# Performance work log

Hardware: AMD Instinct MI355X
Metric: run time of the kernel (lower is better)

The kernel has to match this reference:

```python
import jax, jax.numpy as jnp
import numpy as np


def setup_inputs() -> dict:
    key = jax.random.key(0)
    B, D = 256, 4096
    continuous_input = jax.random.normal(key, (B, D), dtype=jnp.float32)
    return {"continuous_input": continuous_input, "timesteps": 100}


def reference(continuous_input, timesteps):
    # Temporal coding: each (batch, input) pair fires exactly one spike at a
    # time determined by sigmoid(value). With num_neurons == input_dim the
    # neuron index is just the input index, so the scalar scatter in the
    # original nested Python loops is exactly a one-hot over the time axis.
    T = timesteps
    # torch .long() truncates; sigmoid*(T-1) >= 0 so floor == trunc
    spike_times = jnp.floor(jax.nn.sigmoid(continuous_input) * (T - 1)).astype(jnp.int32)  # [B, D]
    t = jnp.arange(T, dtype=jnp.int32)  # [T]
    spikes = (t[:, None, None] == spike_times[None, :, :]).astype(jnp.float32)  # [T, B, N]
    return spikes
```

## Files before the change

### kernel.cpp

```cpp
#include <hip/hip_runtime.h>
#include <math.h>


typedef __attribute__((ext_vector_type(4))) float f32x4;

__device__ __forceinline__ float sigmoidf(float x) {
    return 1.0f / (1.0f + expf(-x));
}

__global__ __launch_bounds__(256) void spike_time_kernel(
    const float* __restrict__ x, unsigned char* __restrict__ st,
    int n, float tm1) {
    const int e = (blockIdx.x * 256 + threadIdx.x) * 4;
    if (e + 3 < n) {
        f32x4 v = *reinterpret_cast<const f32x4*>(x + e);
        uchar4 s;
        s.x = (unsigned char)(int)(sigmoidf(v.x) * tm1);
        s.y = (unsigned char)(int)(sigmoidf(v.y) * tm1);
        s.z = (unsigned char)(int)(sigmoidf(v.z) * tm1);
        s.w = (unsigned char)(int)(sigmoidf(v.w) * tm1);
        *reinterpret_cast<uchar4*>(st + e) = s;
    } else {
        for (int i = e; i < n; ++i)
            st[i] = (unsigned char)(int)(sigmoidf(x[i]) * tm1);
    }
}

__global__ __launch_bounds__(256) void write_onehot_kernel(
    const unsigned char* __restrict__ st, float* __restrict__ out, int n) {
    const int t = blockIdx.y;
    const int e = (blockIdx.x * 256 + threadIdx.x) * 4;
    if (e + 3 < n) {
        uchar4 s = *reinterpret_cast<const uchar4*>(st + e);
        f32x4 o;
        o.x = (s.x == t) ? 1.0f : 0.0f;
        o.y = (s.y == t) ? 1.0f : 0.0f;
        o.z = (s.z == t) ? 1.0f : 0.0f;
        o.w = (s.w == t) ? 1.0f : 0.0f;
        *reinterpret_cast<f32x4*>(out + (size_t)t * n + e) = o;
    } else {
        for (int i = e; i < n; ++i)
            out[(size_t)t * n + i] = (st[i] == t) ? 1.0f : 0.0f;
    }
}

__global__ __launch_bounds__(256) void fused_onehot_kernel(
    const float* __restrict__ x, float* __restrict__ out, int n, float tm1) {
    const int t = blockIdx.y;
    const int e = (blockIdx.x * 256 + threadIdx.x) * 4;
    if (e + 3 < n) {
        f32x4 v = *reinterpret_cast<const f32x4*>(x + e);
        f32x4 o;
        o.x = ((int)(sigmoidf(v.x) * tm1) == t) ? 1.0f : 0.0f;
        o.y = ((int)(sigmoidf(v.y) * tm1) == t) ? 1.0f : 0.0f;
        o.z = ((int)(sigmoidf(v.z) * tm1) == t) ? 1.0f : 0.0f;
        o.w = ((int)(sigmoidf(v.w) * tm1) == t) ? 1.0f : 0.0f;
        *reinterpret_cast<f32x4*>(out + (size_t)t * n + e) = o;
    } else {
        for (int i = e; i < n; ++i)
            out[(size_t)t * n + i] = ((int)(sigmoidf(x[i]) * tm1) == t) ? 1.0f : 0.0f;
    }
}

extern "C" void kernel_launch(void* const* d_in, const int* in_sizes, int n_in,
                              void* d_out, int out_size, void* d_ws, size_t ws_size,
                              hipStream_t stream) {
    const float* x = (const float*)d_in[0];
    float* out = (float*)d_out;
    const int n = in_sizes[0];
    const int T = out_size / n;
    const float tm1 = (float)(T - 1);

    const int n4 = (n + 3) / 4;
    const int blocks_x = (n4 + 255) / 256;

    if (ws_size >= (size_t)n) {
        unsigned char* st = (unsigned char*)d_ws;
        spike_time_kernel<<<blocks_x, 256, 0, stream>>>(x, st, n, tm1);
        dim3 grid(blocks_x, T);
        write_onehot_kernel<<<grid, 256, 0, stream>>>(st, out, n);
    } else {
        dim3 grid(blocks_x, T);
        fused_onehot_kernel<<<grid, 256, 0, stream>>>(x, out, n, tm1);
    }
}
```

Before: 401.6 us.

## Fuse spike-time and one-hot into persistent kernel with nontemporal stores

Replaces the two-kernel path (compute uint8 spike times into workspace, then write one-hot planes) with a single persistent-grid kernel. Each thread computes sigmoid-based spike times for four inputs once and then loops over timesteps, writing float4 one-hot values with nontemporal stores. This removes the workspace round trip and the second launch, and aims to stream the large output efficiently. The fast path requires a power-of-two input size compatible with the fixed grid and otherwise falls back to the per-timestep fused kernel.

```diff
diff --git a/kernel.cpp b/kernel.cpp
--- a/kernel.cpp
+++ b/kernel.cpp
@@ -8,39 +8,31 @@
     return 1.0f / (1.0f + expf(-x));
 }
 
-__global__ __launch_bounds__(256) void spike_time_kernel(
-    const float* __restrict__ x, unsigned char* __restrict__ st,
-    int n, float tm1) {
-    const int e = (blockIdx.x * 256 + threadIdx.x) * 4;
-    if (e + 3 < n) {
-        f32x4 v = *reinterpret_cast<const f32x4*>(x + e);
-        uchar4 s;
-        s.x = (unsigned char)(int)(sigmoidf(v.x) * tm1);
-        s.y = (unsigned char)(int)(sigmoidf(v.y) * tm1);
-        s.z = (unsigned char)(int)(sigmoidf(v.z) * tm1);
-        s.w = (unsigned char)(int)(sigmoidf(v.w) * tm1);
-        *reinterpret_cast<uchar4*>(st + e) = s;
-    } else {
-        for (int i = e; i < n; ++i)
-            st[i] = (unsigned char)(int)(sigmoidf(x[i]) * tm1);
-    }
-}
+__global__ __launch_bounds__(256) void temporal_onehot_fused(
+    const float* __restrict__ x, float* __restrict__ out,
+    int lgp4, int T, float tm1) {
+    const unsigned int S = gridDim.x * 256u;
+    const unsigned int gid = blockIdx.x * 256u + threadIdx.x;
+    const unsigned int mask = (1u << lgp4) - 1u;
+    const unsigned int ci = gid & mask;
+    const unsigned int t0 = gid >> lgp4;
+    const unsigned int tstep = S >> lgp4;
 
-__global__ __launch_bounds__(256) void write_onehot_kernel(
-    const unsigned char* __restrict__ st, float* __restrict__ out, int n) {
-    const int t = blockIdx.y;
-    const int e = (blockIdx.x * 256 + threadIdx.x) * 4;
-    if (e + 3 < n) {
-        uchar4 s = *reinterpret_cast<const uchar4*>(st + e);
+    const f32x4 v = *reinterpret_cast<const f32x4*>(x + (size_t)ci * 4);
+    const int s0 = (int)(sigmoidf(v.x) * tm1);
+    const int s1 = (int)(sigmoidf(v.y) * tm1);
+    const int s2 = (int)(sigmoidf(v.z) * tm1);
+    const int s3 = (int)(sigmoidf(v.w) * tm1);
+
+    f32x4* p = reinterpret_cast<f32x4*>(out) + gid;
+    for (unsigned int t = t0; t < (unsigned int)T; t += tstep) {
         f32x4 o;
-        o.x = (s.x == t) ? 1.0f : 0.0f;
-        o.y = (s.y == t) ? 1.0f : 0.0f;
-        o.z = (s.z == t) ? 1.0f : 0.0f;
-        o.w = (s.w == t) ? 1.0f : 0.0f;
-        *reinterpret_cast<f32x4*>(out + (size_t)t * n + e) = o;
-    } else {
-        for (int i = e; i < n; ++i)
-            out[(size_t)t * n + i] = (st[i] == t) ? 1.0f : 0.0f;
+        o.x = ((int)t == s0) ? 1.0f : 0.0f;
+        o.y = ((int)t == s1) ? 1.0f : 0.0f;
+        o.z = ((int)t == s2) ? 1.0f : 0.0f;
+        o.w = ((int)t == s3) ? 1.0f : 0.0f;
+        __builtin_nontemporal_store(o, p);
+        p += S;
     }
 }
 
@@ -71,15 +63,18 @@
     const int T = out_size / n;
     const float tm1 = (float)(T - 1);
 
-    const int n4 = (n + 3) / 4;
-    const int blocks_x = (n4 + 255) / 256;
-
-    if (ws_size >= (size_t)n) {
-        unsigned char* st = (unsigned char*)d_ws;
-        spike_time_kernel<<<blocks_x, 256, 0, stream>>>(x, st, n, tm1);
-        dim3 grid(blocks_x, T);
-        write_onehot_kernel<<<grid, 256, 0, stream>>>(st, out, n);
+    const bool pow2 = (n & (n - 1)) == 0 && n >= 16;
+    const int blocks = 2048;
+    const unsigned int S = (unsigned int)blocks * 256u;
+    int lgp4 = 0;
+    if (pow2) { while ((4 << lgp4) < n) ++lgp4; }
+    const unsigned int plane_f4 = 1u << lgp4;
+    const bool fast = pow2 && (4 << lgp4) == n &&
+                      S >= plane_f4 && (S % plane_f4) == 0;
+    if (fast) {
+        temporal_onehot_fused<<<blocks, 256, 0, stream>>>(x, out, lgp4, T, tm1);
     } else {
+        const int blocks_x = ((n + 3) / 4 + 255) / 256;
         dim3 grid(blocks_x, T);
         fused_onehot_kernel<<<grid, 256, 0, stream>>>(x, out, n, tm1);
     }
```

New measurement: 429.8 us. 7.0% more time.
